# Kernel tuning notes

Measured on AMD Instinct MI355X. Metric: run time of the kernel, lower is better.

Reference implementation:

```python
import jax, jax.numpy as jnp
import numpy as np


def _attention(q, v):
    # q: [N, d] (q == k), v: [N, Dv]. Non-standard: scaled scores get +1 bias
    # before softmax (constant shift -> no effect on softmax, but kept faithful).
    d = q.shape[-1]
    scores = (q @ q.T) / jnp.sqrt(jnp.asarray(d, q.dtype)) + 1.0  # [N, N]
    w = jax.nn.softmax(scores, axis=-1)
    return w @ v


def setup_inputs() -> dict:
    key = jax.random.key(0)
    ks = jax.random.split(key, 9)
    N_REVIEW, N_USER, N_ITEM, D, K, OUT = 16384, 8192, 8192, 32, 4, 64
    IN_DIM = K * (D + D)  # 256
    return {
        "review_vecs": jax.random.normal(ks[0], (N_REVIEW, D), jnp.float32),
        "user_vecs": jax.random.normal(ks[1], (N_USER, D), jnp.float32),
        "item_vecs": jax.random.normal(ks[2], (N_ITEM, D), jnp.float32),
        "adj_ur": jax.random.randint(ks[3], (N_USER, K), 0, N_REVIEW),
        "adj_ri": jax.random.randint(ks[4], (N_USER, K), 0, N_ITEM),
        "adj_ir": jax.random.randint(ks[5], (N_ITEM, K), 0, N_REVIEW),
        "adj_ru": jax.random.randint(ks[6], (N_ITEM, K), 0, N_USER),
        "user_neigh_W": jax.random.normal(ks[7], (IN_DIM, OUT), jnp.float32) * 0.05,
        "item_neigh_W": jax.random.normal(ks[8], (IN_DIM, OUT), jnp.float32) * 0.05,
    }


def reference(review_vecs, user_vecs, item_vecs, adj_ur, adj_ri, adj_ir, adj_ru,
              user_neigh_W, item_neigh_W):
    # dropout=0.0 -> identity; tf.random.shuffle permutes the feature axis
    # randomly -> identity permutation used as the deterministic reference.
    Nu, Ni = user_vecs.shape[0], item_vecs.shape[0]
    ur = review_vecs[adj_ur]            # [Nu, K, Dr]
    ri = item_vecs[adj_ri]              # [Nu, K, Di]
    ir = review_vecs[adj_ir]            # [Ni, K, Dr]
    ru = user_vecs[adj_ru]              # [Ni, K, Du]
    cat_user = jnp.concatenate([ur, ri], axis=2).reshape(Nu, -1)  # [Nu, K*(Dr+Di)]
    cat_item = jnp.concatenate([ir, ru], axis=2).reshape(Ni, -1)  # [Ni, K*(Dr+Du)]
    user_agg = _attention(user_vecs, cat_user)  # [Nu, IN_DIM]
    item_agg = _attention(item_vecs, cat_item)  # [Ni, IN_DIM]
    user_out = jax.nn.relu(user_agg @ user_neigh_W)  # [Nu, OUT]
    item_out = jax.nn.relu(item_agg @ item_neigh_W)  # [Ni, OUT]
    return user_out, item_out
```

## Files before the change

### kernel.cpp

```cpp
#include <hip/hip_runtime.h>
#include <math.h>

#define NR 8192
#define DQ 32
#define DV 256
#define OUT_DIM 64
#define NSPLIT 4
#define BK 64
#define NIT ((NR / NSPLIT) / BK)
#define QSCALE2 0.5050114839784955f

typedef short short4v __attribute__((ext_vector_type(4)));
typedef short short8 __attribute__((ext_vector_type(8)));
typedef float f32x16 __attribute__((ext_vector_type(16)));
typedef unsigned int u32;
typedef __attribute__((address_space(1))) const u32 gas_t;
typedef __attribute__((address_space(3))) u32 las_t;

__device__ __forceinline__ unsigned short f32_to_bf16(float f) {
    union { float f; unsigned int u; } v; v.f = f;
    unsigned int u = v.u + 0x7FFFu + ((v.u >> 16) & 1u);
    return (unsigned short)(u >> 16);
}
__device__ __forceinline__ float exp2_fast(float x) {
#if __has_builtin(__builtin_amdgcn_exp2f)
    return __builtin_amdgcn_exp2f(x);
#else
    return exp2f(x);
#endif
}

__global__ void prep_kernel(
        const float* __restrict__ review,
        const float* __restrict__ user,
        const float* __restrict__ item,
        const int* __restrict__ adj_ur, const int* __restrict__ adj_ri,
        const int* __restrict__ adj_ir, const int* __restrict__ adj_ru,
        const float* __restrict__ Wu,  const float* __restrict__ Wi,
        unsigned short* __restrict__ qh,
        unsigned short* __restrict__ wbf,
        unsigned short* __restrict__ vt) {
    __shared__ __align__(16) unsigned short T[64][264];
    int b = blockIdx.x, t = threadIdx.x;
    if (b < 256) {
        int side = b >> 7;
        int bxg  = b & 127;
        int key0 = bxg * 64;
        const int* adjA   = side ? adj_ir : adj_ur;
        const int* adjB   = side ? adj_ru : adj_ri;
        const float* srcB = side ? user : item;
        {
            int key = t >> 2, q = t & 3;
#pragma unroll
            for (int rr = 0; rr < 2; ++rr) {
                int ss  = q * 2 + rr;
                int knb = ss >> 1, isB = ss & 1;
                int row = (isB ? adjB : adjA)[(key0 + key) * 4 + knb];
                const float4* src = (const float4*)((isB ? srcB : review) + (size_t)row * DQ);
                int dbase = knb * 64 + isB * 32;
#pragma unroll
                for (int d = 0; d < 4; ++d) {
                    float4 a = src[d * 2], b2 = src[d * 2 + 1];
                    short8 v;
                    v[0] = (short)f32_to_bf16(a.x);  v[1] = (short)f32_to_bf16(a.y);
                    v[2] = (short)f32_to_bf16(a.z);  v[3] = (short)f32_to_bf16(a.w);
                    v[4] = (short)f32_to_bf16(b2.x); v[5] = (short)f32_to_bf16(b2.y);
                    v[6] = (short)f32_to_bf16(b2.z); v[7] = (short)f32_to_bf16(b2.w);
                    *(short8*)&T[key][dbase + d * 8] = v;
                }
            }
        }
        __syncthreads();
#pragma unroll
        for (int w8 = 0; w8 < 8; ++w8) {
            int u    = t + 256 * w8;
            int g    = u >> 9;
            int ct   = (u >> 6) & 7;
            int lane = u & 63;
            int ln = lane & 31, h = lane >> 5;
            int kt = g >> 1, a = g & 1;
            int col = ct * 32 + ln;
            short8 v;
#pragma unroll
            for (int i = 0; i < 8; ++i) {
                int lkey = kt * 32 + a * 16 + h * 4 + 8 * (i >> 2) + (i & 3);
                v[i] = (short)T[lkey][col];
            }
            size_t dst = (size_t)side * NR * DV + (size_t)bxg * 16384 + (size_t)u * 8;
            *(short8*)(vt + dst) = v;
        }
        return;
    }
    b -= 256;
    if (b < 512) {
        int i = (b * 256 + t) * 4;
        int side  = i >= NR * DQ;
        int local = i - side * NR * DQ;
        const float* src = side ? item : user;
        float4 v = *(const float4*)(src + local);
        short4v o;
        o[0] = (short)f32_to_bf16(v.x * QSCALE2);
        o[1] = (short)f32_to_bf16(v.y * QSCALE2);
        o[2] = (short)f32_to_bf16(v.z * QSCALE2);
        o[3] = (short)f32_to_bf16(v.w * QSCALE2);
        *(short4v*)(qh + i) = o;
        return;
    }
    b -= 512;
    int g  = b * 256 + t;
    int ln = g & 31, h = (g >> 5) & 1, nt = (g >> 6) & 1;
    int kt = (g >> 7) & 3, p = (g >> 9) & 3, wm = g >> 11;
    const float* W = wm ? Wi : Wu;
    unsigned short* dst = wbf + (size_t)g * 8;
#pragma unroll
    for (int i = 0; i < 8; ++i) {
        int k = p * 64 + kt * 16 + h * 8 + i;
        dst[i] = f32_to_bf16(W[k * OUT_DIM + nt * 32 + ln]);
    }
}

__global__ __launch_bounds__(256, 2) void flash_kernel(
        const unsigned short* __restrict__ qh,
        const unsigned short* __restrict__ vt,
        const unsigned short* __restrict__ wbf,
        float* __restrict__ opart,
        float* __restrict__ lpart)
{
    const int bx   = blockIdx.x;
    const int side = bx & 1;
    const int sp   = (bx >> 1) & (NSPLIT - 1);
    const int rb   = bx >> 3;
    const int w    = threadIdx.x >> 6;
    const int lane = threadIdx.x & 63;
    const int ln   = lane & 31;
    const int h    = lane >> 5;

    const int m0 = rb * 128 + w * 32;
    const unsigned short* Q  = qh + (size_t)side * NR * DQ;
    const unsigned short* VT = vt + (size_t)side * NR * DV;
    const int t64_0 = sp * NIT;

    __shared__ __align__(16) unsigned short Vbuf[2][16384];
    unsigned short* Ew = &Vbuf[0][0] + w * (32 * 72);

    auto stage = [&](int tile, int b) {
        const unsigned short* src = VT + (size_t)tile * 16384 + w * 4096 + lane * 8;
        unsigned short* dst = &Vbuf[b][w * 4096];
#pragma unroll
        for (int k2 = 0; k2 < 8; ++k2)
            __builtin_amdgcn_global_load_lds((gas_t*)(src + k2 * 512),
                                             (las_t*)(dst + k2 * 512), 16, 0, 0);
    };
    auto load_ka = [&](int j0, short8* ka) {
#pragma unroll
        for (int kt = 0; kt < 2; ++kt)
#pragma unroll
            for (int dh = 0; dh < 2; ++dh)
                ka[kt * 2 + dh] = *(const short8*)(Q + (size_t)(j0 + kt * 32 + ln) * DQ
                                                   + dh * 16 + h * 8);
    };

    short8 bq[2];
#pragma unroll
    for (int dh = 0; dh < 2; ++dh)
        bq[dh] = *(const short8*)(Q + (size_t)(m0 + ln) * DQ + dh * 16 + h * 8);

    f32x16 zf;
#pragma unroll
    for (int r = 0; r < 16; ++r) zf[r] = 0.f;
    f32x16 o[8];
#pragma unroll
    for (int ct = 0; ct < 8; ++ct) o[ct] = zf;
    float l_acc = 0.f;

    short8 fr[4];
    short8 ka_buf[4];

    auto exp_chunk = [&](const f32x16& Cs, int g) {
        int a = g & 1;
        union { short8 s; u32 u[4]; } f;
#pragma unroll
        for (int j = 0; j < 4; ++j) {
            float e0 = exp2_fast(Cs[8 * a + 2 * j]);
            float e1 = exp2_fast(Cs[8 * a + 2 * j + 1]);
            l_acc += e0 + e1;
            u32 u0 = __builtin_bit_cast(u32, e0) + 0x8000u;
            u32 u1 = __builtin_bit_cast(u32, e1) + 0x8000u;
            f.u[j] = __builtin_amdgcn_perm(u1, u0, 0x07060302);
        }
        fr[g] = f.s;
    };

    {
        load_ka(t64_0 * 64, ka_buf);
        stage(t64_0, 0);
        f32x16 c0 = __builtin_amdgcn_mfma_f32_32x32x16_bf16(ka_buf[0], bq[0], zf, 0, 0, 0);
        c0 = __builtin_amdgcn_mfma_f32_32x32x16_bf16(ka_buf[1], bq[1], c0, 0, 0, 0);
        f32x16 c1 = __builtin_amdgcn_mfma_f32_32x32x16_bf16(ka_buf[2], bq[0], zf, 0, 0, 0);
        c1 = __builtin_amdgcn_mfma_f32_32x32x16_bf16(ka_buf[3], bq[1], c1, 0, 0, 0);
        exp_chunk(c0, 0); exp_chunk(c0, 1);
        exp_chunk(c1, 2); exp_chunk(c1, 3);
        load_ka(t64_0 * 64 + BK, ka_buf);
    }
    __syncthreads();

    for (int it = 0; it < NIT; ++it) {
        const int more = (it + 1 < NIT);
        f32x16 C0, C1;
        if (more) {
            stage(t64_0 + it + 1, (it + 1) & 1);
            if (it + 2 < NIT) {
                short8 ka_nx[4];
                load_ka((t64_0 + it + 2) * 64, ka_nx);
                C0 = __builtin_amdgcn_mfma_f32_32x32x16_bf16(ka_buf[0], bq[0], zf, 0, 0, 0);
                C0 = __builtin_amdgcn_mfma_f32_32x32x16_bf16(ka_buf[1], bq[1], C0, 0, 0, 0);
                C1 = __builtin_amdgcn_mfma_f32_32x32x16_bf16(ka_buf[2], bq[0], zf, 0, 0, 0);
                C1 = __builtin_amdgcn_mfma_f32_32x32x16_bf16(ka_buf[3], bq[1], C1, 0, 0, 0);
                ka_buf[0] = ka_nx[0]; ka_buf[1] = ka_nx[1];
                ka_buf[2] = ka_nx[2]; ka_buf[3] = ka_nx[3];
            } else {
                C0 = __builtin_amdgcn_mfma_f32_32x32x16_bf16(ka_buf[0], bq[0], zf, 0, 0, 0);
                C0 = __builtin_amdgcn_mfma_f32_32x32x16_bf16(ka_buf[1], bq[1], C0, 0, 0, 0);
                C1 = __builtin_amdgcn_mfma_f32_32x32x16_bf16(ka_buf[2], bq[0], zf, 0, 0, 0);
                C1 = __builtin_amdgcn_mfma_f32_32x32x16_bf16(ka_buf[3], bq[1], C1, 0, 0, 0);
            }
        }
        const unsigned short* vb = &Vbuf[it & 1][0] + (size_t)lane * 8;
#pragma unroll
        for (int g = 0; g < 4; ++g) {
#pragma unroll
            for (int ct = 0; ct < 8; ++ct) {
                short8 bv = *(const short8*)(vb + (g * 8 + ct) * 512);
                o[ct] = __builtin_amdgcn_mfma_f32_32x32x16_bf16(fr[g], bv, o[ct], 0, 0, 0);
            }
            if (more) exp_chunk((g < 2) ? C0 : C1, g);
        }
        if (more) __syncthreads();
    }

    l_acc += __shfl_xor(l_acc, 32);
    if (h == 0)
        lpart[(size_t)(sp * 2 + side) * NR + m0 + ln] = l_acc;

    f32x16 pp[2];
    pp[0] = zf; pp[1] = zf;
    const unsigned short* wb_base = wbf + (size_t)side * 16384;
#pragma unroll
    for (int p = 0; p < 4; ++p) {
        __builtin_amdgcn_s_waitcnt(0xC07F);
#pragma unroll
        for (int c2 = 0; c2 < 2; ++c2)
#pragma unroll
            for (int r = 0; r < 16; ++r) {
                int row = (r & 3) + ((r >> 2) << 3) + h * 4;
                Ew[row * 72 + c2 * 32 + ln] = f32_to_bf16(o[2 * p + c2][r]);
            }
#pragma unroll
        for (int kt = 0; kt < 4; ++kt) {
            short8 a = *(const short8*)&Ew[ln * 72 + kt * 16 + h * 8];
#pragma unroll
            for (int nt = 0; nt < 2; ++nt) {
                short8 bw = *(const short8*)(wb_base
                            + ((size_t)(p * 4 + kt) * 2 + nt) * 512 + (size_t)lane * 8);
                pp[nt] = __builtin_amdgcn_mfma_f32_32x32x16_bf16(a, bw, pp[nt], 0, 0, 0);
            }
        }
    }

    float* op = opart + ((size_t)(sp * 2 + side) * NR + m0) * OUT_DIM;
#pragma unroll
    for (int nt = 0; nt < 2; ++nt)
#pragma unroll
        for (int r = 0; r < 16; ++r) {
            int row = (r & 3) + ((r >> 2) << 3) + h * 4;
            op[(size_t)row * OUT_DIM + nt * 32 + ln] = pp[nt][r];
        }
}

__global__ void final_kernel(const float4* __restrict__ opart,
                             const float* __restrict__ lpart,
                             float4* __restrict__ out) {
    int i4  = blockIdx.x * blockDim.x + threadIdx.x;
    int row = i4 >> 4;
    float4 v = make_float4(0.f, 0.f, 0.f, 0.f);
    float L = 0.f;
#pragma unroll
    for (int sp = 0; sp < NSPLIT; ++sp) {
        float4 a = opart[(size_t)sp * (2 * NR * 16) + i4];
        v.x += a.x; v.y += a.y; v.z += a.z; v.w += a.w;
        L += lpart[(size_t)sp * (2 * NR) + row];
    }
    float inv = 1.0f / L;
    out[i4] = make_float4(fmaxf(v.x * inv, 0.f), fmaxf(v.y * inv, 0.f),
                          fmaxf(v.z * inv, 0.f), fmaxf(v.w * inv, 0.f));
}

extern "C" void kernel_launch(void* const* d_in, const int* in_sizes, int n_in,
                              void* d_out, int out_size, void* d_ws, size_t ws_size,
                              hipStream_t stream) {
    const float* review = (const float*)d_in[0];
    const float* user   = (const float*)d_in[1];
    const float* item   = (const float*)d_in[2];
    const int* adj_ur   = (const int*)d_in[3];
    const int* adj_ri   = (const int*)d_in[4];
    const int* adj_ir   = (const int*)d_in[5];
    const int* adj_ru   = (const int*)d_in[6];
    const float* Wu     = (const float*)d_in[7];
    const float* Wi     = (const float*)d_in[8];
    float* out = (float*)d_out;

    float* opart = (float*)d_ws;
    float* lpart = opart + (size_t)NSPLIT * 2 * NR * OUT_DIM;
    unsigned short* vt  = (unsigned short*)(lpart + (size_t)NSPLIT * 2 * NR);
    unsigned short* qh  = vt + (size_t)2 * NR * DV;
    unsigned short* wbf = qh + (size_t)2 * NR * DQ;

    prep_kernel<<<784, 256, 0, stream>>>(
        review, user, item, adj_ur, adj_ri, adj_ir, adj_ru, Wu, Wi,
        qh, wbf, vt);
    flash_kernel<<<512, 256, 0, stream>>>(qh, vt, wbf, opart, lpart);
    final_kernel<<<1024, 256, 0, stream>>>((const float4*)opart, lpart, (float4*)out);
}
```

Measured before the change: 155.8 us.

## Fuse prep, flash attention and final reduce into one cooperative kernel

Replaces the three-kernel launch sequence with a single cooperative kernel of 256 blocks of 512 threads. Grid-wide syncs separate the bf16 conversion and gather phase, the flash attention with projection phase, and the split reduction phase. Each flash block now covers 256 rows with 8 waves instead of 128 rows. The goal is to remove inter-kernel launch gaps and tail effects. In exchange the grid shrinks to 256 blocks, which may underfill the GPU, and it adds grid-barrier cost, with the old three-kernel path kept as a fallback if the cooperative launch fails.

```diff
diff --git a/kernel.cpp b/kernel.cpp
--- a/kernel.cpp
+++ b/kernel.cpp
@@ -1,5 +1,8 @@
 #include <hip/hip_runtime.h>
+#include <hip/hip_cooperative_groups.h>
 #include <math.h>
+
+namespace cg = cooperative_groups;
 
 #define NR 8192
 #define DQ 32
@@ -28,6 +31,276 @@
 #else
     return exp2f(x);
 #endif
+}
+
+__global__ __launch_bounds__(512, 2) void fused_kernel(
+        const float* __restrict__ review,
+        const float* __restrict__ user,
+        const float* __restrict__ item,
+        const int* __restrict__ adj_ur, const int* __restrict__ adj_ri,
+        const int* __restrict__ adj_ir, const int* __restrict__ adj_ru,
+        const float* __restrict__ Wu,  const float* __restrict__ Wi,
+        unsigned short* __restrict__ qh,
+        unsigned short* __restrict__ wbf,
+        unsigned short* __restrict__ vt,
+        float* __restrict__ opart,
+        float* __restrict__ lpart,
+        float* __restrict__ out)
+{
+    cg::grid_group grid = cg::this_grid();
+    const int bx = blockIdx.x;
+    const int t  = threadIdx.x;
+
+    __shared__ __align__(16) unsigned short smem[32768];
+
+    {
+        int i = (bx * 512 + t) * 4;
+        int qside = i >= NR * DQ;
+        int local = i - qside * NR * DQ;
+        const float* qsrc = qside ? item : user;
+        float4 qv = *(const float4*)(qsrc + local);
+        short4v qo;
+        qo[0] = (short)f32_to_bf16(qv.x * QSCALE2);
+        qo[1] = (short)f32_to_bf16(qv.y * QSCALE2);
+        qo[2] = (short)f32_to_bf16(qv.z * QSCALE2);
+        qo[3] = (short)f32_to_bf16(qv.w * QSCALE2);
+        *(short4v*)(qh + i) = qo;
+
+        if (bx < 8) {
+            int g  = bx * 512 + t;
+            int ln = g & 31, h2 = (g >> 5) & 1, nt = (g >> 6) & 1;
+            int kt = (g >> 7) & 3, p = (g >> 9) & 3, wm = g >> 11;
+            const float* W = wm ? Wi : Wu;
+            unsigned short* dst = wbf + (size_t)g * 8;
+#pragma unroll
+            for (int i8 = 0; i8 < 8; ++i8) {
+                int k = p * 64 + kt * 16 + h2 * 8 + i8;
+                dst[i8] = f32_to_bf16(W[k * OUT_DIM + nt * 32 + ln]);
+            }
+        }
+
+        unsigned short (*T)[264] = (unsigned short(*)[264])smem;
+        int side = bx >> 7;
+        int bxg  = bx & 127;
+        int key0 = bxg * 64;
+        const int* adjA   = side ? adj_ir : adj_ur;
+        const int* adjB   = side ? adj_ru : adj_ri;
+        const float* srcB = side ? user : item;
+        {
+            int key = t >> 3, ss = t & 7;
+            int knb = ss >> 1, isB = ss & 1;
+            int row = (isB ? adjB : adjA)[(key0 + key) * 4 + knb];
+            const float4* src = (const float4*)((isB ? srcB : review) + (size_t)row * DQ);
+            int dbase = knb * 64 + isB * 32;
+#pragma unroll
+            for (int d = 0; d < 4; ++d) {
+                float4 a = src[d * 2], b2 = src[d * 2 + 1];
+                short8 v;
+                v[0] = (short)f32_to_bf16(a.x);  v[1] = (short)f32_to_bf16(a.y);
+                v[2] = (short)f32_to_bf16(a.z);  v[3] = (short)f32_to_bf16(a.w);
+                v[4] = (short)f32_to_bf16(b2.x); v[5] = (short)f32_to_bf16(b2.y);
+                v[6] = (short)f32_to_bf16(b2.z); v[7] = (short)f32_to_bf16(b2.w);
+                *(short8*)&T[key][dbase + d * 8] = v;
+            }
+        }
+        __syncthreads();
+#pragma unroll
+        for (int w8 = 0; w8 < 4; ++w8) {
+            int u    = t + 512 * w8;
+            int g    = u >> 9;
+            int ct   = (u >> 6) & 7;
+            int lane = u & 63;
+            int ln = lane & 31, h2 = lane >> 5;
+            int kt = g >> 1, a = g & 1;
+            int col = ct * 32 + ln;
+            short8 v;
+#pragma unroll
+            for (int i8 = 0; i8 < 8; ++i8) {
+                int lkey = kt * 32 + a * 16 + h2 * 4 + 8 * (i8 >> 2) + (i8 & 3);
+                v[i8] = (short)T[lkey][col];
+            }
+            size_t dst = (size_t)side * NR * DV + (size_t)bxg * 16384 + (size_t)u * 8;
+            *(short8*)(vt + dst) = v;
+        }
+    }
+
+    grid.sync();
+
+    {
+        const int side = bx & 1;
+        const int sp   = (bx >> 1) & (NSPLIT - 1);
+        const int rb   = bx >> 3;
+        const int w    = t >> 6;
+        const int lane = t & 63;
+        const int ln   = lane & 31;
+        const int h    = lane >> 5;
+
+        const int m0 = rb * 256 + w * 32;
+        const unsigned short* Q  = qh + (size_t)side * NR * DQ;
+        const unsigned short* VT = vt + (size_t)side * NR * DV;
+        const int t64_0 = sp * NIT;
+
+        unsigned short* Vb0 = smem;
+        unsigned short* Vb1 = smem + 16384;
+        unsigned short* Ew = smem + w * (32 * 72);
+
+        auto stage = [&](int tile, int b) {
+            const unsigned short* src = VT + (size_t)tile * 16384 + w * 2048 + lane * 8;
+            unsigned short* dst = (b ? Vb1 : Vb0) + w * 2048;
+#pragma unroll
+            for (int k2 = 0; k2 < 4; ++k2)
+                __builtin_amdgcn_global_load_lds((gas_t*)(src + k2 * 512),
+                                                 (las_t*)(dst + k2 * 512), 16, 0, 0);
+        };
+        auto load_ka = [&](int j0, short8* ka) {
+#pragma unroll
+            for (int kt = 0; kt < 2; ++kt)
+#pragma unroll
+                for (int dh = 0; dh < 2; ++dh)
+                    ka[kt * 2 + dh] = *(const short8*)(Q + (size_t)(j0 + kt * 32 + ln) * DQ
+                                                       + dh * 16 + h * 8);
+        };
+
+        short8 bq[2];
+#pragma unroll
+        for (int dh = 0; dh < 2; ++dh)
+            bq[dh] = *(const short8*)(Q + (size_t)(m0 + ln) * DQ + dh * 16 + h * 8);
+
+        f32x16 zf;
+#pragma unroll
+        for (int r = 0; r < 16; ++r) zf[r] = 0.f;
+        f32x16 o[8];
+#pragma unroll
+        for (int ct = 0; ct < 8; ++ct) o[ct] = zf;
+        float l_acc = 0.f;
+
+        short8 fr[4];
+        short8 ka_buf[4];
+
+        auto exp_chunk = [&](const f32x16& Cs, int g) {
+            int a = g & 1;
+            union { short8 s; u32 u[4]; } f;
+#pragma unroll
+            for (int j = 0; j < 4; ++j) {
+                float e0 = exp2_fast(Cs[8 * a + 2 * j]);
+                float e1 = exp2_fast(Cs[8 * a + 2 * j + 1]);
+                l_acc += e0 + e1;
+                u32 u0 = __builtin_bit_cast(u32, e0) + 0x8000u;
+                u32 u1 = __builtin_bit_cast(u32, e1) + 0x8000u;
+                f.u[j] = __builtin_amdgcn_perm(u1, u0, 0x07060302);
+            }
+            fr[g] = f.s;
+        };
+
+        {
+            load_ka(t64_0 * 64, ka_buf);
+            stage(t64_0, 0);
+            f32x16 c0 = __builtin_amdgcn_mfma_f32_32x32x16_bf16(ka_buf[0], bq[0], zf, 0, 0, 0);
+            c0 = __builtin_amdgcn_mfma_f32_32x32x16_bf16(ka_buf[1], bq[1], c0, 0, 0, 0);
+            f32x16 c1 = __builtin_amdgcn_mfma_f32_32x32x16_bf16(ka_buf[2], bq[0], zf, 0, 0, 0);
+            c1 = __builtin_amdgcn_mfma_f32_32x32x16_bf16(ka_buf[3], bq[1], c1, 0, 0, 0);
+            exp_chunk(c0, 0); exp_chunk(c0, 1);
+            exp_chunk(c1, 2); exp_chunk(c1, 3);
+            load_ka(t64_0 * 64 + BK, ka_buf);
+        }
+        __syncthreads();
+
+        for (int it = 0; it < NIT; ++it) {
+            const int more = (it + 1 < NIT);
+            f32x16 C0, C1;
+            if (more) {
+                stage(t64_0 + it + 1, (it + 1) & 1);
+                if (it + 2 < NIT) {
+                    short8 ka_nx[4];
+                    load_ka((t64_0 + it + 2) * 64, ka_nx);
+                    C0 = __builtin_amdgcn_mfma_f32_32x32x16_bf16(ka_buf[0], bq[0], zf, 0, 0, 0);
+                    C0 = __builtin_amdgcn_mfma_f32_32x32x16_bf16(ka_buf[1], bq[1], C0, 0, 0, 0);
+                    C1 = __builtin_amdgcn_mfma_f32_32x32x16_bf16(ka_buf[2], bq[0], zf, 0, 0, 0);
+                    C1 = __builtin_amdgcn_mfma_f32_32x32x16_bf16(ka_buf[3], bq[1], C1, 0, 0, 0);
+                    ka_buf[0] = ka_nx[0]; ka_buf[1] = ka_nx[1];
+                    ka_buf[2] = ka_nx[2]; ka_buf[3] = ka_nx[3];
+                } else {
+                    C0 = __builtin_amdgcn_mfma_f32_32x32x16_bf16(ka_buf[0], bq[0], zf, 0, 0, 0);
+                    C0 = __builtin_amdgcn_mfma_f32_32x32x16_bf16(ka_buf[1], bq[1], C0, 0, 0, 0);
+                    C1 = __builtin_amdgcn_mfma_f32_32x32x16_bf16(ka_buf[2], bq[0], zf, 0, 0, 0);
+                    C1 = __builtin_amdgcn_mfma_f32_32x32x16_bf16(ka_buf[3], bq[1], C1, 0, 0, 0);
+                }
+            }
+            const unsigned short* vb = (it & 1 ? Vb1 : Vb0) + (size_t)lane * 8;
+#pragma unroll
+            for (int g = 0; g < 4; ++g) {
+#pragma unroll
+                for (int ct = 0; ct < 8; ++ct) {
+                    short8 bv = *(const short8*)(vb + (g * 8 + ct) * 512);
+                    o[ct] = __builtin_amdgcn_mfma_f32_32x32x16_bf16(fr[g], bv, o[ct], 0, 0, 0);
+                }
+                if (more) exp_chunk((g < 2) ? C0 : C1, g);
+            }
+            if (more) __syncthreads();
+        }
+        __syncthreads();
+
+        l_acc += __shfl_xor(l_acc, 32);
+        if (h == 0)
+            lpart[(size_t)(sp * 2 + side) * NR + m0 + ln] = l_acc;
+
+        f32x16 pp[2];
+        pp[0] = zf; pp[1] = zf;
+        const unsigned short* wb_base = wbf + (size_t)side * 16384;
+#pragma unroll
+        for (int p = 0; p < 4; ++p) {
+            __builtin_amdgcn_s_waitcnt(0xC07F);
+#pragma unroll
+            for (int c2 = 0; c2 < 2; ++c2)
+#pragma unroll
+                for (int r = 0; r < 16; ++r) {
+                    int row = (r & 3) + ((r >> 2) << 3) + h * 4;
+                    Ew[row * 72 + c2 * 32 + ln] = f32_to_bf16(o[2 * p + c2][r]);
+                }
+#pragma unroll
+            for (int kt = 0; kt < 4; ++kt) {
+                short8 a = *(const short8*)&Ew[ln * 72 + kt * 16 + h * 8];
+#pragma unroll
+                for (int nt = 0; nt < 2; ++nt) {
+                    short8 bw = *(const short8*)(wb_base
+                                + ((size_t)(p * 4 + kt) * 2 + nt) * 512 + (size_t)lane * 8);
+                    pp[nt] = __builtin_amdgcn_mfma_f32_32x32x16_bf16(a, bw, pp[nt], 0, 0, 0);
+                }
+            }
+        }
+
+        float* op = opart + ((size_t)(sp * 2 + side) * NR + m0) * OUT_DIM;
+#pragma unroll
+        for (int nt = 0; nt < 2; ++nt)
+#pragma unroll
+            for (int r = 0; r < 16; ++r) {
+                int row = (r & 3) + ((r >> 2) << 3) + h * 4;
+                op[(size_t)row * OUT_DIM + nt * 32 + ln] = pp[nt][r];
+            }
+    }
+
+    grid.sync();
+
+    {
+        const float4* op4 = (const float4*)opart;
+        float4* out4 = (float4*)out;
+#pragma unroll
+        for (int rep = 0; rep < 2; ++rep) {
+            int i4  = (bx * 512 + t) * 2 + rep;
+            int row = i4 >> 4;
+            float4 v = make_float4(0.f, 0.f, 0.f, 0.f);
+            float L = 0.f;
+#pragma unroll
+            for (int sp = 0; sp < NSPLIT; ++sp) {
+                float4 a = op4[(size_t)sp * (2 * NR * 16) + i4];
+                v.x += a.x; v.y += a.y; v.z += a.z; v.w += a.w;
+                L += lpart[(size_t)sp * (2 * NR) + row];
+            }
+            float inv = 1.0f / L;
+            out4[i4] = make_float4(fmaxf(v.x * inv, 0.f), fmaxf(v.y * inv, 0.f),
+                                   fmaxf(v.z * inv, 0.f), fmaxf(v.w * inv, 0.f));
+        }
+    }
 }
 
 __global__ void prep_kernel(
@@ -77,14 +350,14 @@
             int g    = u >> 9;
             int ct   = (u >> 6) & 7;
             int lane = u & 63;
-            int ln = lane & 31, h = lane >> 5;
+            int ln = lane & 31, h2 = lane >> 5;
             int kt = g >> 1, a = g & 1;
             int col = ct * 32 + ln;
             short8 v;
 #pragma unroll
-            for (int i = 0; i < 8; ++i) {
-                int lkey = kt * 32 + a * 16 + h * 4 + 8 * (i >> 2) + (i & 3);
-                v[i] = (short)T[lkey][col];
+            for (int i8 = 0; i8 < 8; ++i8) {
+                int lkey = kt * 32 + a * 16 + h2 * 4 + 8 * (i8 >> 2) + (i8 & 3);
+                v[i8] = (short)T[lkey][col];
             }
             size_t dst = (size_t)side * NR * DV + (size_t)bxg * 16384 + (size_t)u * 8;
             *(short8*)(vt + dst) = v;
@@ -108,14 +381,14 @@
     }
     b -= 512;
     int g  = b * 256 + t;
-    int ln = g & 31, h = (g >> 5) & 1, nt = (g >> 6) & 1;
+    int ln = g & 31, h2 = (g >> 5) & 1, nt = (g >> 6) & 1;
     int kt = (g >> 7) & 3, p = (g >> 9) & 3, wm = g >> 11;
     const float* W = wm ? Wi : Wu;
     unsigned short* dst = wbf + (size_t)g * 8;
 #pragma unroll
-    for (int i = 0; i < 8; ++i) {
-        int k = p * 64 + kt * 16 + h * 8 + i;
-        dst[i] = f32_to_bf16(W[k * OUT_DIM + nt * 32 + ln]);
+    for (int i8 = 0; i8 < 8; ++i8) {
+        int k = p * 64 + kt * 16 + h2 * 8 + i8;
+        dst[i8] = f32_to_bf16(W[k * OUT_DIM + nt * 32 + ln]);
     }
 }
 
@@ -315,9 +588,22 @@
     unsigned short* qh  = vt + (size_t)2 * NR * DV;
     unsigned short* wbf = qh + (size_t)2 * NR * DQ;
 
-    prep_kernel<<<784, 256, 0, stream>>>(
-        review, user, item, adj_ur, adj_ri, adj_ir, adj_ru, Wu, Wi,
-        qh, wbf, vt);
-    flash_kernel<<<512, 256, 0, stream>>>(qh, vt, wbf, opart, lpart);
-    final_kernel<<<1024, 256, 0, stream>>>((const float4*)opart, lpart, (float4*)out);
+    void* args[] = {
+        (void*)&review, (void*)&user, (void*)&item,
+        (void*)&adj_ur, (void*)&adj_ri, (void*)&adj_ir, (void*)&adj_ru,
+        (void*)&Wu, (void*)&Wi,
+        (void*)&qh, (void*)&wbf, (void*)&vt,
+        (void*)&opart, (void*)&lpart, (void*)&out
+    };
+    hipError_t err = hipLaunchCooperativeKernel((void*)fused_kernel,
+                                                dim3(256), dim3(512),
+                                                args, 0, stream);
+    if (err != hipSuccess) {
+        prep_kernel<<<784, 256, 0, stream>>>(
+            review, user, item, adj_ur, adj_ri, adj_ir, adj_ru, Wu, Wi,
+            qh, wbf, vt);
+        flash_kernel<<<512, 256, 0, stream>>>(qh, vt, wbf, opart, lpart);
+        final_kernel<<<1024, 256, 0, stream>>>((const float4*)opart, lpart,
+                                               (float4*)out);
+    }
 }
```

New measurement: 243.8 us. +56.5%, slower.

## Fuse split-K reduction into flash kernel via last-block atomic counter

Applied to the files above, without the earlier changes.

Removes the separate final reduction kernel. Each flash block bumps a per-row-block atomic counter after writing its partial results, and the last of the NSPLIT blocks to finish sums the partials, normalizes, applies ReLU and writes the output. The counters are zeroed by an extra block in the prep kernel. This saves one kernel launch and its scheduling gap, at the cost of a threadfence, an atomic and a serialized reduction tail in some blocks.

```diff
diff --git a/kernel.cpp b/kernel.cpp
--- a/kernel.cpp
+++ b/kernel.cpp
@@ -39,7 +39,8 @@
         const float* __restrict__ Wu,  const float* __restrict__ Wi,
         unsigned short* __restrict__ qh,
         unsigned short* __restrict__ wbf,
-        unsigned short* __restrict__ vt) {
+        unsigned short* __restrict__ vt,
+        int* __restrict__ done) {
     __shared__ __align__(16) unsigned short T[64][264];
     int b = blockIdx.x, t = threadIdx.x;
     if (b < 256) {
@@ -77,14 +78,14 @@
             int g    = u >> 9;
             int ct   = (u >> 6) & 7;
             int lane = u & 63;
-            int ln = lane & 31, h = lane >> 5;
+            int ln = lane & 31, h2 = lane >> 5;
             int kt = g >> 1, a = g & 1;
             int col = ct * 32 + ln;
             short8 v;
 #pragma unroll
-            for (int i = 0; i < 8; ++i) {
-                int lkey = kt * 32 + a * 16 + h * 4 + 8 * (i >> 2) + (i & 3);
-                v[i] = (short)T[lkey][col];
+            for (int i8 = 0; i8 < 8; ++i8) {
+                int lkey = kt * 32 + a * 16 + h2 * 4 + 8 * (i8 >> 2) + (i8 & 3);
+                v[i8] = (short)T[lkey][col];
             }
             size_t dst = (size_t)side * NR * DV + (size_t)bxg * 16384 + (size_t)u * 8;
             *(short8*)(vt + dst) = v;
@@ -107,16 +108,20 @@
         return;
     }
     b -= 512;
-    int g  = b * 256 + t;
-    int ln = g & 31, h = (g >> 5) & 1, nt = (g >> 6) & 1;
-    int kt = (g >> 7) & 3, p = (g >> 9) & 3, wm = g >> 11;
-    const float* W = wm ? Wi : Wu;
-    unsigned short* dst = wbf + (size_t)g * 8;
-#pragma unroll
-    for (int i = 0; i < 8; ++i) {
-        int k = p * 64 + kt * 16 + h * 8 + i;
-        dst[i] = f32_to_bf16(W[k * OUT_DIM + nt * 32 + ln]);
-    }
+    if (b < 16) {
+        int g  = b * 256 + t;
+        int ln = g & 31, h2 = (g >> 5) & 1, nt = (g >> 6) & 1;
+        int kt = (g >> 7) & 3, p = (g >> 9) & 3, wm = g >> 11;
+        const float* W = wm ? Wi : Wu;
+        unsigned short* dst = wbf + (size_t)g * 8;
+#pragma unroll
+        for (int i8 = 0; i8 < 8; ++i8) {
+            int k = p * 64 + kt * 16 + h2 * 8 + i8;
+            dst[i8] = f32_to_bf16(W[k * OUT_DIM + nt * 32 + ln]);
+        }
+        return;
+    }
+    if (t < 128) done[t] = 0;
 }
 
 __global__ __launch_bounds__(256, 2) void flash_kernel(
@@ -124,7 +129,9 @@
         const unsigned short* __restrict__ vt,
         const unsigned short* __restrict__ wbf,
         float* __restrict__ opart,
-        float* __restrict__ lpart)
+        float* __restrict__ lpart,
+        int* __restrict__ done,
+        float* __restrict__ out)
 {
     const int bx   = blockIdx.x;
     const int side = bx & 1;
@@ -141,6 +148,7 @@
     const int t64_0 = sp * NIT;
 
     __shared__ __align__(16) unsigned short Vbuf[2][16384];
+    __shared__ int last_flag;
     unsigned short* Ew = &Vbuf[0][0] + w * (32 * 72);
 
     auto stage = [&](int tile, int b) {
@@ -275,24 +283,39 @@
             int row = (r & 3) + ((r >> 2) << 3) + h * 4;
             op[(size_t)row * OUT_DIM + nt * 32 + ln] = pp[nt][r];
         }
-}
-
-__global__ void final_kernel(const float4* __restrict__ opart,
-                             const float* __restrict__ lpart,
-                             float4* __restrict__ out) {
-    int i4  = blockIdx.x * blockDim.x + threadIdx.x;
-    int row = i4 >> 4;
-    float4 v = make_float4(0.f, 0.f, 0.f, 0.f);
-    float L = 0.f;
-#pragma unroll
-    for (int sp = 0; sp < NSPLIT; ++sp) {
-        float4 a = opart[(size_t)sp * (2 * NR * 16) + i4];
-        v.x += a.x; v.y += a.y; v.z += a.z; v.w += a.w;
-        L += lpart[(size_t)sp * (2 * NR) + row];
-    }
-    float inv = 1.0f / L;
-    out[i4] = make_float4(fmaxf(v.x * inv, 0.f), fmaxf(v.y * inv, 0.f),
-                          fmaxf(v.z * inv, 0.f), fmaxf(v.w * inv, 0.f));
+
+    __threadfence();
+    __syncthreads();
+    if (threadIdx.x == 0) {
+        int old = atomicAdd(&done[side * 64 + rb], 1);
+        last_flag = (old == NSPLIT - 1);
+    }
+    __syncthreads();
+    if (last_flag) {
+        __threadfence();
+        const float4* op4 = (const float4*)opart;
+        float4* out4 = (float4*)out;
+#pragma unroll
+        for (int k = 0; k < 8; ++k) {
+            int idx   = threadIdx.x + 256 * k;
+            int row_l = idx >> 4;
+            int c4    = idx & 15;
+            int row   = rb * 128 + row_l;
+            float4 v = make_float4(0.f, 0.f, 0.f, 0.f);
+            float L = 0.f;
+#pragma unroll
+            for (int s2 = 0; s2 < NSPLIT; ++s2) {
+                size_t i4 = ((size_t)(s2 * 2 + side) * NR + row) * 16 + c4;
+                float4 a = op4[i4];
+                v.x += a.x; v.y += a.y; v.z += a.z; v.w += a.w;
+                L += lpart[(size_t)(s2 * 2 + side) * NR + row];
+            }
+            float inv = 1.0f / L;
+            out4[((size_t)side * NR + row) * 16 + c4] =
+                make_float4(fmaxf(v.x * inv, 0.f), fmaxf(v.y * inv, 0.f),
+                            fmaxf(v.z * inv, 0.f), fmaxf(v.w * inv, 0.f));
+        }
+    }
 }
 
 extern "C" void kernel_launch(void* const* d_in, const int* in_sizes, int n_in,
@@ -314,10 +337,10 @@
     unsigned short* vt  = (unsigned short*)(lpart + (size_t)NSPLIT * 2 * NR);
     unsigned short* qh  = vt + (size_t)2 * NR * DV;
     unsigned short* wbf = qh + (size_t)2 * NR * DQ;
-
-    prep_kernel<<<784, 256, 0, stream>>>(
+    int* done = (int*)(wbf + 32768);
+
+    prep_kernel<<<785, 256, 0, stream>>>(
         review, user, item, adj_ur, adj_ri, adj_ir, adj_ru, Wu, Wi,
-        qh, wbf, vt);
-    flash_kernel<<<512, 256, 0, stream>>>(qh, vt, wbf, opart, lpart);
-    final_kernel<<<1024, 256, 0, stream>>>((const float4*)opart, lpart, (float4*)out);
-}
+        qh, wbf, vt, done);
+    flash_kernel<<<512, 256, 0, stream>>>(qh, vt, wbf, opart, lpart, done, out);
+}
```

Measured after the change: 247.2 us. +58.7%, slower.
